# Kernel optimization log

Hardware: AMD Instinct MI355X
Metric: run time of the kernel (lower is better)

Reference implementation:

```python
import jax, jax.numpy as jnp
import numpy as np

B, N_PROP = 2, 512
C_FEAT, FH, FW = 256, 200, 200
NUM_CLASSES, NUM_STAGES = 81, 3
POOL, SR, SCALE = 7, 2, 0.25
IMG_H, IMG_W = 800.0, 800.0
FC_DIM = 1024
IN_DIM = C_FEAT * POOL * POOL
STDS = ((0.1, 0.1, 0.2, 0.2), (0.05, 0.05, 0.1, 0.1), (0.033, 0.033, 0.067, 0.067))
CLIP_VAL = float(np.log(1000.0 / 16))
SCORE_T, NMS_T, DETS, PRE_NMS = 0.05, 0.5, 100, 2048


def bilinear(f, y, x):
    # f: [C,H,W]; y,x: [M] sample coords (torchvision roi_align bilinear rules)
    H, W = f.shape[1], f.shape[2]
    valid = (y > -1.0) & (y < H) & (x > -1.0) & (x < W)
    y = jnp.clip(y, 0.0, H - 1.0)
    x = jnp.clip(x, 0.0, W - 1.0)
    y0 = jnp.floor(y).astype(jnp.int32)
    x0 = jnp.floor(x).astype(jnp.int32)
    y1 = jnp.minimum(y0 + 1, H - 1)
    x1 = jnp.minimum(x0 + 1, W - 1)
    ly, lx = y - y0, x - x0
    hy, hx = 1.0 - ly, 1.0 - lx
    v = (hy * hx) * f[:, y0, x0] + (hy * lx) * f[:, y0, x1] \
      + (ly * hx) * f[:, y1, x0] + (ly * lx) * f[:, y1, x1]
    return v * valid  # [C,M]


def roi_align(f, rois):
    # f: [C,H,W], rois: [N,4] image coords -> [N,C,POOL,POOL]
    b = rois * SCALE
    x1, y1, x2, y2 = b[:, 0], b[:, 1], b[:, 2], b[:, 3]
    rw = jnp.maximum(x2 - x1, 1.0)
    rh = jnp.maximum(y2 - y1, 1.0)
    bw, bh = rw / POOL, rh / POOL
    p = jnp.arange(POOL, dtype=f.dtype)
    s = (jnp.arange(SR, dtype=f.dtype) + 0.5) / SR
    gy = y1[:, None, None] + (p[None, :, None] + s[None, None, :]) * bh[:, None, None]  # [N,P,SR]
    gx = x1[:, None, None] + (p[None, :, None] + s[None, None, :]) * bw[:, None, None]
    n = rois.shape[0]
    yy = jnp.broadcast_to(gy[:, :, :, None, None], (n, POOL, SR, POOL, SR))
    xx = jnp.broadcast_to(gx[:, None, None, :, :], (n, POOL, SR, POOL, SR))
    vals = bilinear(f, yy.reshape(-1), xx.reshape(-1))  # [C, N*P*SR*P*SR]
    vals = vals.reshape(f.shape[0], n, POOL, SR, POOL, SR).mean(axis=(3, 5))
    return vals.transpose(1, 0, 2, 3)


def decode_clip(props, deltas, stds):
    px1, py1, px2, py2 = props[:, 0], props[:, 1], props[:, 2], props[:, 3]
    pw = jnp.maximum(px2 - px1, 1e-6)
    ph = jnp.maximum(py2 - py1, 1e-6)
    px = px1 + 0.5 * pw
    py = py1 + 0.5 * ph
    wx, wy, ww, wh = stds
    dx = deltas[:, 0] * wx
    dy = deltas[:, 1] * wy
    dw = jnp.minimum(deltas[:, 2] * ww, CLIP_VAL)
    dh = jnp.minimum(deltas[:, 3] * wh, CLIP_VAL)
    gx = dx * pw + px
    gy = dy * ph + py
    gw = jnp.exp(dw) * pw
    gh = jnp.exp(dh) * ph
    return jnp.stack([jnp.clip(gx - 0.5 * gw, 0.0, IMG_W),
                      jnp.clip(gy - 0.5 * gh, 0.0, IMG_H),
                      jnp.clip(gx + 0.5 * gw, 0.0, IMG_W),
                      jnp.clip(gy + 0.5 * gh, 0.0, IMG_H)], axis=1)


def box_iou(a, b):
    area_a = (a[:, 2] - a[:, 0]) * (a[:, 3] - a[:, 1])
    area_b = (b[:, 2] - b[:, 0]) * (b[:, 3] - b[:, 1])
    lt = jnp.maximum(a[:, None, :2], b[None, :, :2])
    rb = jnp.minimum(a[:, None, 2:], b[None, :, 2:])
    wh = jnp.maximum(rb - lt, 0.0)
    inter = wh[..., 0] * wh[..., 1]
    return inter / (area_a[:, None] + area_b[None, :] - inter + 1e-12)


def postprocess(boxes, probs):
    # boxes [N,4], probs [N,NUM_CLASSES] -> fixed-size padded detections
    n = boxes.shape[0]
    ws = boxes[:, 2] - boxes[:, 0]
    hs = boxes[:, 3] - boxes[:, 1]
    ok = (ws >= 1.0) & (hs >= 1.0)  # remove_small_boxes(min_size=1.0)
    fg = probs[:, 1:]               # drop background (class 0)
    sc = jnp.where((fg > SCORE_T) & ok[:, None], fg, -1.0).reshape(-1)  # [N*(C-1)]
    labels = jnp.broadcast_to(jnp.arange(1, NUM_CLASSES, dtype=jnp.int32)[None, :],
                              (n, NUM_CLASSES - 1)).reshape(-1)
    bflat = jnp.broadcast_to(boxes[:, None, :], (n, NUM_CLASSES - 1, 4)).reshape(-1, 4)
    vals, idx = jax.lax.top_k(sc, PRE_NMS)  # fixed-size candidate cap, sorted desc
    bsel = bflat[idx]
    lsel = labels[idx]
    # batched_nms trick: offset boxes per label so classes never overlap
    off = bsel + (lsel.astype(bsel.dtype) * (jnp.max(bsel) + 1.0))[:, None]
    iou = box_iou(off, off)
    valid = vals > 0.0
    ar = jnp.arange(PRE_NMS)
    def body(i, keep):
        sup = (iou[i] > NMS_T) & keep[i]
        return keep & ~(sup & (ar > i))
    keep = jax.lax.fori_loop(0, PRE_NMS, body, valid)
    order = jnp.argsort(jnp.where(keep, ar, PRE_NMS + ar))[:DETS]  # kept first, score order
    kv = keep[order]
    out_boxes = jnp.where(kv[:, None], bsel[order], 0.0)
    out_scores = jnp.where(kv, vals[order], 0.0)
    out_labels = jnp.where(kv, lsel[order], 0)
    return out_boxes, out_scores, out_labels


def cascade_forward(features, proposals, W1, b1, W2, b2, Wc, bc, Wr, br):
    cur = proposals  # [B,N,4]
    logits = None
    for s in range(NUM_STAGES):
        pooled = jax.vmap(roi_align)(features, cur)  # [B,N,C,P,P]
        x = pooled.reshape(B * N_PROP, IN_DIM)
        h = jax.nn.relu(x @ W1[s] + b1[s])
        h = jax.nn.relu(h @ W2[s] + b2[s])
        logits = h @ Wc[s] + bc[s]
        deltas = (h @ Wr[s] + br[s]).reshape(B, N_PROP, 4)
        stds = STDS[s]
        cur = jax.vmap(lambda p, d: decode_clip(p, d, stds))(cur, deltas)
    probs = jax.nn.softmax(logits, axis=-1).reshape(B, N_PROP, NUM_CLASSES)
    return jax.vmap(postprocess)(cur, probs)


def setup_inputs() -> dict:
    key = jax.random.key(0)
    ks = jax.random.split(key, 12)
    features = jax.random.normal(ks[0], (B, C_FEAT, FH, FW), jnp.float32)
    cx = jax.random.uniform(ks[1], (B, N_PROP), minval=0.0, maxval=IMG_W)
    cy = jax.random.uniform(ks[2], (B, N_PROP), minval=0.0, maxval=IMG_H)
    w = jax.random.uniform(ks[3], (B, N_PROP), minval=16.0, maxval=256.0)
    h = jax.random.uniform(ks[4], (B, N_PROP), minval=16.0, maxval=256.0)
    proposals = jnp.stack([jnp.clip(cx - w / 2, 0.0, IMG_W), jnp.clip(cy - h / 2, 0.0, IMG_H),
                           jnp.clip(cx + w / 2, 0.0, IMG_W), jnp.clip(cy + h / 2, 0.0, IMG_H)],
                          axis=-1)
    def lin(k, fan_in, shape):
        return jax.random.normal(k, shape, jnp.float32) / np.sqrt(fan_in).astype(np.float32)
    W1 = lin(ks[5], IN_DIM, (NUM_STAGES, IN_DIM, FC_DIM))
    W2 = lin(ks[6], FC_DIM, (NUM_STAGES, FC_DIM, FC_DIM))
    Wc = lin(ks[7], FC_DIM, (NUM_STAGES, FC_DIM, NUM_CLASSES))
    Wr = lin(ks[8], FC_DIM, (NUM_STAGES, FC_DIM, 4)) * 0.5
    b1 = jnp.zeros((NUM_STAGES, FC_DIM), jnp.float32)
    b2 = jnp.zeros((NUM_STAGES, FC_DIM), jnp.float32)
    bc = jnp.zeros((NUM_STAGES, NUM_CLASSES), jnp.float32)
    br = jnp.zeros((NUM_STAGES, 4), jnp.float32)
    return {"features": features, "proposals": proposals, "W1": W1, "b1": b1,
            "W2": W2, "b2": b2, "Wc": Wc, "bc": bc, "Wr": Wr, "br": br}


def reference(features, proposals, W1, b1, W2, b2, Wc, bc, Wr, br):
    return cascade_forward(features, proposals, W1, b1, W2, b2, Wc, bc, Wr, br)
```

## Files before the change

kernel.cpp:

```cpp
#include <hip/hip_runtime.h>
#include <float.h>
#include <math.h>

#define NB 2
#define NPROP 512
#define NROI 1024
#define CFEAT 256
#define FH 200
#define FW 200
#define HWSZ 40000
#define INDIM 12544
#define FCD 1024
#define NCLS 81
#define NCAND 40960
#define CAP 4096
#define NSEL 2048
#define DETS 100
#define CLIPV 4.135166556742356f

#define KKT1 392
#define KKT2 32
#define SPLITK 8

typedef __attribute__((ext_vector_type(8))) short short8v;
typedef __attribute__((ext_vector_type(8))) unsigned short ushort8v;
typedef __attribute__((ext_vector_type(4))) float float4v;

__device__ __forceinline__ unsigned short f2bf(float x) {
    unsigned u = __float_as_uint(x);
    unsigned r = (u + 0x7fffu + ((u >> 16) & 1u)) >> 16;
    return (unsigned short)r;
}
__device__ __forceinline__ float bf2f(unsigned short b) {
    return __uint_as_float(((unsigned)b) << 16);
}
__device__ __forceinline__ void split3(float x, unsigned short& h, unsigned short& m, unsigned short& l) {
    h = f2bf(x);
    float r1 = x - bf2f(h);
    m = f2bf(r1);
    float r2 = r1 - bf2f(m);
    l = f2bf(r2);
}

__device__ __forceinline__ void gload_lds16(const void* g, void* l) {
    __builtin_amdgcn_global_load_lds((const __attribute__((address_space(1))) unsigned int*)g,
                                     (__attribute__((address_space(3))) unsigned int*)l, 16, 0, 0);
}

__device__ __forceinline__ int swz8k(int o) {
    return o ^ ((((o >> 6) ^ (o >> 8)) & 3) << 4);
}

__global__ void zero_ints_k(int* p, int n) {
    int i = blockIdx.x * blockDim.x + threadIdx.x;
    if (i < n) p[i] = 0;
}

__global__ __launch_bounds__(256) void transpose_k(const float* __restrict__ in, float* __restrict__ out) {
    __shared__ float tile[32][33];
    int b = blockIdx.z;
    int hw0 = blockIdx.x * 32;
    int c0 = blockIdx.y * 32;
    int tx = threadIdx.x;
    int ty = threadIdx.y;
#pragma unroll
    for (int i = 0; i < 32; i += 8)
        tile[ty + i][tx] = in[((size_t)(b * CFEAT + c0 + ty + i)) * HWSZ + hw0 + tx];
    __syncthreads();
#pragma unroll
    for (int i = 0; i < 32; i += 8)
        out[((size_t)b * HWSZ + hw0 + ty + i) * CFEAT + c0 + tx] = tile[tx][ty + i];
}

template<bool TRANS>
__device__ __forceinline__ float bil_sample(const float* __restrict__ feat, int b, int c,
                                            float yy, float xx) {
    bool valid = (yy > -1.f) && (yy < (float)FH) && (xx > -1.f) && (xx < (float)FW);
    float yc = fminf(fmaxf(yy, 0.f), (float)(FH - 1));
    float xc = fminf(fmaxf(xx, 0.f), (float)(FW - 1));
    int y0 = (int)floorf(yc), x0 = (int)floorf(xc);
    int y1i = min(y0 + 1, FH - 1), x1i = min(x0 + 1, FW - 1);
    float ly = yc - (float)y0, lx = xc - (float)x0;
    float hy = 1.f - ly, hx = 1.f - lx;
    float v00, v01, v10, v11;
    if (TRANS) {
        const float* base = feat + (size_t)b * HWSZ * CFEAT;
        v00 = base[((size_t)(y0 * FW + x0)) * CFEAT + c];
        v01 = base[((size_t)(y0 * FW + x1i)) * CFEAT + c];
        v10 = base[((size_t)(y1i * FW + x0)) * CFEAT + c];
        v11 = base[((size_t)(y1i * FW + x1i)) * CFEAT + c];
    } else {
        const float* base = feat + ((size_t)(b * CFEAT + c)) * HWSZ;
        v00 = base[y0 * FW + x0];
        v01 = base[y0 * FW + x1i];
        v10 = base[y1i * FW + x0];
        v11 = base[y1i * FW + x1i];
    }
    float v = hy * hx * v00 + hy * lx * v01 + ly * hx * v10 + ly * lx * v11;
    return valid ? v : 0.f;
}

template<bool TRANS>
__global__ __launch_bounds__(256) void roi_k(const float* __restrict__ feat,
                                             const float* __restrict__ boxes,
                                             float* __restrict__ xout) {
    int pp = blockIdx.x, r = blockIdx.y, c = threadIdx.x;
    int b = r >> 9;
    const float* bx = boxes + (size_t)r * 4;
    float x1 = bx[0] * 0.25f, y1 = bx[1] * 0.25f, x2 = bx[2] * 0.25f, y2 = bx[3] * 0.25f;
    float rw = fmaxf(x2 - x1, 1.0f), rh = fmaxf(y2 - y1, 1.0f);
    float bw = rw / 7.0f, bh = rh / 7.0f;
    int py = pp / 7, px = pp % 7;
    float acc = 0.f;
#pragma unroll
    for (int sy = 0; sy < 2; ++sy)
#pragma unroll
        for (int sx = 0; sx < 2; ++sx)
            acc += bil_sample<TRANS>(feat, b, c,
                                     y1 + ((float)py + 0.25f + 0.5f * (float)sy) * bh,
                                     x1 + ((float)px + 0.25f + 0.5f * (float)sx) * bw);
    xout[(size_t)r * INDIM + pp * 256 + c] = acc * 0.25f;
}

template<bool TRANS>
__global__ __launch_bounds__(256) void roi_split_k(const float* __restrict__ feat,
                                                   const float* __restrict__ boxes,
                                                   unsigned short* __restrict__ Ap) {
    int r = blockIdx.x;
    int c = threadIdx.x;
    int b = r >> 9;
    const float* bx = boxes + (size_t)r * 4;
    float x1 = bx[0] * 0.25f, y1 = bx[1] * 0.25f, x2 = bx[2] * 0.25f, y2 = bx[3] * 0.25f;
    float rw = fmaxf(x2 - x1, 1.0f), rh = fmaxf(y2 - y1, 1.0f);
    float bw = rw / 7.0f, bh = rh / 7.0f;
    int mt = r >> 7, rr = r & 127;
    size_t pstr = (size_t)8 * KKT1 * 4096;
    for (int pp = 0; pp < 49; ++pp) {
        int py = pp / 7, px = pp % 7;
        float acc = 0.f;
#pragma unroll
        for (int sy = 0; sy < 2; ++sy)
#pragma unroll
            for (int sx = 0; sx < 2; ++sx)
                acc += bil_sample<TRANS>(feat, b, c,
                                         y1 + ((float)py + 0.25f + 0.5f * (float)sy) * bh,
                                         x1 + ((float)px + 0.25f + 0.5f * (float)sx) * bw);
        acc *= 0.25f;
        unsigned short h, m, l;
        split3(acc, h, m, l);
        int k = pp * 256 + c;
        int kk = k >> 5;
        size_t tile = ((size_t)mt * KKT1 + kk) * 4096 + rr * 32 + (k & 31);
        Ap[tile] = h;
        Ap[tile + pstr] = m;
        Ap[tile + 2 * pstr] = l;
    }
}

template<bool PERM>
__global__ __launch_bounds__(256) void wsplit_k(const float* __restrict__ W,
                                                unsigned short* __restrict__ out, int kkT) {
    __shared__ float tf[32][132];
    int nt = blockIdx.x, kk = blockIdx.y;
    int t = threadIdx.x;
    int kloc = t >> 3;
    int f4 = t & 7;
    int krow;
    if (PERM) krow = ((kk & 7) * 32 + kloc) * 49 + (kk >> 3);
    else krow = kk * 32 + kloc;
    const float* src = W + (size_t)krow * 1024 + nt * 128;
#pragma unroll
    for (int q = 0; q < 4; ++q) {
        float4 v = *(const float4*)(src + (f4 + q * 8) * 4);
        *(float4*)&tf[kloc][(f4 + q * 8) * 4] = v;
    }
    __syncthreads();
    int r = t >> 1;
    size_t tileBase = ((size_t)nt * kkT + kk) * 4096;
    size_t pstr = (size_t)8 * kkT * 4096;
#pragma unroll
    for (int cc = 0; cc < 2; ++cc) {
        int c = (t & 1) * 2 + cc;
        ushort8v hv, mv, lv;
#pragma unroll
        for (int e = 0; e < 8; ++e) {
            unsigned short h, m, l;
            split3(tf[c * 8 + e][r], h, m, l);
            hv[e] = h; mv[e] = m; lv[e] = l;
        }
        size_t o = tileBase + r * 32 + c * 8;
        *(ushort8v*)&out[o] = hv;
        *(ushort8v*)&out[o + pstr] = mv;
        *(ushort8v*)&out[o + 2 * pstr] = lv;
    }
}

#define TERM16(AF) { _Pragma("unroll") for (int i = 0; i < 4; ++i) _Pragma("unroll") \
    for (int j = 0; j < 4; ++j) acc[i][j] = __builtin_amdgcn_mfma_f32_16x16x32_bf16(AF[i], bf[j], acc[i][j], 0, 0, 0); }

__global__ __launch_bounds__(256) void gemm_mfma_k(const unsigned short* __restrict__ Ap,
                                                   const unsigned short* __restrict__ Bp,
                                                   float* __restrict__ partial,
                                                   int kkT, int kkPer) {
    __shared__ unsigned short sA[3][4096];
    __shared__ unsigned short sB[3][4096];
    int tid = threadIdx.x;
    int phys = blockIdx.x;
    int logical = (phys & 7) * (gridDim.x >> 3) + (phys >> 3);
    int xy = logical & 63;
    int ck = logical >> 6;
    int mt = xy & 7, nt = xy >> 3;
    int kk0 = ck * kkPer;
    size_t pstrB = (size_t)8 * kkT * 4096 * 2;
    const char* aBase = (const char*)(Ap + (size_t)mt * kkT * 4096);
    const char* bBase = (const char*)(Bp + (size_t)nt * kkT * 4096);

    float4v acc[4][4];
#pragma unroll
    for (int i = 0; i < 4; ++i)
#pragma unroll
        for (int j = 0; j < 4; ++j) acc[i][j] = (float4v){0.f, 0.f, 0.f, 0.f};

    int lane = tid & 63, wv = tid >> 6;
    int wr = wv >> 1, wc = wv & 1;
    int ln = lane & 15;
    int q = lane >> 4;
    int qs = (q ^ (ln ^ (ln >> 2))) & 3;
    int aoffE = (wr * 64 + ln) * 32 + qs * 8;
    int boffE = (wc * 64 + ln) * 32 + qs * 8;

    int o0 = tid * 16;
    int o1 = o0 + 4096;
    int s0 = swz8k(o0);
    int s1 = swz8k(o1);

    for (int kk = kk0; kk < kk0 + kkPer; ++kk) {
        const char* at = aBase + (size_t)kk * 8192;
        const char* bt = bBase + (size_t)kk * 8192;
#pragma unroll
        for (int p = 0; p < 3; ++p) {
            gload_lds16(at + (size_t)p * pstrB + s0, (char*)sA[p] + o0);
            gload_lds16(at + (size_t)p * pstrB + s1, (char*)sA[p] + o1);
            gload_lds16(bt + (size_t)p * pstrB + s0, (char*)sB[p] + o0);
            gload_lds16(bt + (size_t)p * pstrB + s1, (char*)sB[p] + o1);
        }
        __syncthreads();
        short8v af[3][4];
#pragma unroll
        for (int p = 0; p < 3; ++p)
#pragma unroll
            for (int f = 0; f < 4; ++f)
                af[p][f] = *(const short8v*)&sA[p][aoffE + f * 512];
        short8v bf[4];
#pragma unroll
        for (int f = 0; f < 4; ++f) bf[f] = *(const short8v*)&sB[0][boffE + f * 512];
        TERM16(af[0]); TERM16(af[1]); TERM16(af[2]);
#pragma unroll
        for (int f = 0; f < 4; ++f) bf[f] = *(const short8v*)&sB[1][boffE + f * 512];
        TERM16(af[0]); TERM16(af[1]);
#pragma unroll
        for (int f = 0; f < 4; ++f) bf[f] = *(const short8v*)&sB[2][boffE + f * 512];
        TERM16(af[0]);
        __syncthreads();
    }
    float* outp = partial + ((size_t)ck << 20);
    int row0 = mt * 128 + wr * 64 + (lane >> 4) * 4;
    int col = nt * 128 + wc * 64 + ln;
#pragma unroll
    for (int i = 0; i < 4; ++i)
#pragma unroll
        for (int j = 0; j < 4; ++j)
#pragma unroll
            for (int qq = 0; qq < 4; ++qq)
                outp[(size_t)(row0 + i * 16 + qq) * 1024 + col + j * 16] = acc[i][j][qq];
}

template<int MODE>
__global__ void reduce8_k(const float* __restrict__ partial, const float* __restrict__ bias,
                          unsigned short* __restrict__ planes, float* __restrict__ fout) {
    int i = blockIdx.x * 256 + threadIdx.x;
    float s = 0.f;
#pragma unroll
    for (int c = 0; c < SPLITK; ++c) s += partial[((size_t)c << 20) + i];
    s += bias[i & 1023];
    s = fmaxf(s, 0.f);
    if (MODE == 0) {
        int m = i >> 10, n = i & 1023;
        int mt = m >> 7, rr = m & 127, kk = n >> 5;
        unsigned short h, mm_, l;
        split3(s, h, mm_, l);
        size_t tile = ((size_t)mt * KKT2 + kk) * 4096 + rr * 32 + (n & 31);
        size_t pstr = (size_t)8 * KKT2 * 4096;
        planes[tile] = h;
        planes[tile + pstr] = mm_;
        planes[tile + 2 * pstr] = l;
    } else {
        fout[i] = s;
    }
}

template<bool PERM>
__global__ __launch_bounds__(256) void gemm_k(const float* __restrict__ A,
                                              const float* __restrict__ Bm,
                                              float* __restrict__ partial,
                                              int K_total, int Kchunk) {
    const int M = 1024, N = 1024;
    __shared__ float As[2][16][128];
    __shared__ float Bs[2][16][64];
    int tid = threadIdx.x;
    int mb = blockIdx.x & 7;
    int nb = blockIdx.x >> 3;
    int ck = blockIdx.y;
    int k0 = ck * Kchunk;
    int am = tid >> 1;
    int ak = (tid & 1) * 8;
    int bk = tid >> 4;
    int bn = (tid & 15) * 4;
    int ty = tid >> 4, tx = tid & 15;
    const float* Aptr = A + (size_t)(mb * 128 + am) * K_total + k0 + ak;

    float acc[8][4];
#pragma unroll
    for (int i = 0; i < 8; ++i)
#pragma unroll
        for (int j = 0; j < 4; ++j) acc[i][j] = 0.f;

    auto bRowPtr = [&](int kk) -> const float* {
        int row = PERM ? ((kk & 255) * 49 + (kk >> 8)) : kk;
        return Bm + (size_t)row * N + nb * 64 + bn;
    };

    int T = Kchunk / 16;
    float4 a0 = *(const float4*)(Aptr);
    float4 a1 = *(const float4*)(Aptr + 4);
    float4 b0 = *(const float4*)bRowPtr(k0 + bk);
    As[0][ak + 0][am] = a0.x; As[0][ak + 1][am] = a0.y; As[0][ak + 2][am] = a0.z; As[0][ak + 3][am] = a0.w;
    As[0][ak + 4][am] = a1.x; As[0][ak + 5][am] = a1.y; As[0][ak + 6][am] = a1.z; As[0][ak + 7][am] = a1.w;
    *(float4*)&Bs[0][bk][bn] = b0;
    __syncthreads();

    int p = 0;
    for (int t = 0; t < T; ++t) {
        if (t + 1 < T) {
            a0 = *(const float4*)(Aptr + (t + 1) * 16);
            a1 = *(const float4*)(Aptr + (t + 1) * 16 + 4);
            b0 = *(const float4*)bRowPtr(k0 + (t + 1) * 16 + bk);
        }
#pragma unroll
        for (int k = 0; k < 16; ++k) {
            float4 av0 = *(const float4*)&As[p][k][ty * 8];
            float4 av1 = *(const float4*)&As[p][k][ty * 8 + 4];
            float4 bv = *(const float4*)&Bs[p][k][tx * 4];
            float ar[8] = {av0.x, av0.y, av0.z, av0.w, av1.x, av1.y, av1.z, av1.w};
            float br_[4] = {bv.x, bv.y, bv.z, bv.w};
#pragma unroll
            for (int i = 0; i < 8; ++i)
#pragma unroll
                for (int j = 0; j < 4; ++j) acc[i][j] = fmaf(ar[i], br_[j], acc[i][j]);
        }
        if (t + 1 < T) {
            __syncthreads();
            int qb = 1 - p;
            As[qb][ak + 0][am] = a0.x; As[qb][ak + 1][am] = a0.y; As[qb][ak + 2][am] = a0.z; As[qb][ak + 3][am] = a0.w;
            As[qb][ak + 4][am] = a1.x; As[qb][ak + 5][am] = a1.y; As[qb][ak + 6][am] = a1.z; As[qb][ak + 7][am] = a1.w;
            *(float4*)&Bs[qb][bk][bn] = b0;
            __syncthreads();
            p = qb;
        }
    }
    float* out = partial + ((size_t)ck * M + mb * 128 + ty * 8) * N + nb * 64 + tx * 4;
#pragma unroll
    for (int i = 0; i < 8; ++i) {
        float4 v = make_float4(acc[i][0], acc[i][1], acc[i][2], acc[i][3]);
        *(float4*)(out + (size_t)i * N) = v;
    }
}

__global__ void reduce4_k(const float* __restrict__ partial, const float* __restrict__ bias,
                          float* __restrict__ out) {
    const int MN = 1024 * 1024;
    int i = blockIdx.x * 256 + threadIdx.x;
    if (i >= MN) return;
    float s = partial[i] + partial[(size_t)MN + i] + partial[(size_t)2 * MN + i] + partial[(size_t)3 * MN + i];
    s += bias[i & 1023];
    out[i] = fmaxf(s, 0.f);
}

__global__ __launch_bounds__(128) void head_k(const float* __restrict__ h,
                                              const float* __restrict__ Wc, const float* __restrict__ bc,
                                              const float* __restrict__ Wr, const float* __restrict__ br,
                                              float* __restrict__ logits, float* __restrict__ deltas,
                                              int write_logits) {
    __shared__ float hs[1024];
    int m = blockIdx.x;
    int tid = threadIdx.x;
    const float4* hp = (const float4*)(h + (size_t)m * 1024);
    ((float4*)hs)[tid] = hp[tid];
    ((float4*)hs)[tid + 128] = hp[tid + 128];
    __syncthreads();
    int j = tid;
    if (j < 85) {
        bool is_cls = j < 81;
        const float* Wp = is_cls ? Wc : Wr;
        int stride = is_cls ? 81 : 4;
        int col = is_cls ? j : j - 81;
        float s0 = 0.f, s1 = 0.f, s2 = 0.f, s3 = 0.f;
        for (int k = 0; k < 1024; k += 4) {
            s0 = fmaf(hs[k + 0], Wp[(k + 0) * stride + col], s0);
            s1 = fmaf(hs[k + 1], Wp[(k + 1) * stride + col], s1);
            s2 = fmaf(hs[k + 2], Wp[(k + 2) * stride + col], s2);
            s3 = fmaf(hs[k + 3], Wp[(k + 3) * stride + col], s3);
        }
        float s = (s0 + s1) + (s2 + s3);
        if (is_cls) {
            if (write_logits) logits[(size_t)m * NCLS + col] = s + bc[col];
        } else {
            deltas[(size_t)m * 4 + col] = s + br[col];
        }
    }
}

__global__ void decode_k(const float* __restrict__ prev, const float* __restrict__ deltas,
                         float* __restrict__ nxt, float wx, float wy, float ww, float wh) {
    int r = blockIdx.x * 256 + threadIdx.x;
    if (r >= NROI) return;
    const float* p = prev + (size_t)r * 4;
    const float* d = deltas + (size_t)r * 4;
    float px1 = p[0], py1 = p[1], px2 = p[2], py2 = p[3];
    float pw = fmaxf(px2 - px1, 1e-6f), ph = fmaxf(py2 - py1, 1e-6f);
    float pcx = px1 + 0.5f * pw, pcy = py1 + 0.5f * ph;
    float dx = d[0] * wx, dy = d[1] * wy;
    float dw = fminf(d[2] * ww, CLIPV);
    float dh = fminf(d[3] * wh, CLIPV);
    float gx = dx * pw + pcx, gy = dy * ph + pcy;
    float gw = expf(dw) * pw, gh = expf(dh) * ph;
    nxt[(size_t)r * 4 + 0] = fminf(fmaxf(gx - 0.5f * gw, 0.f), 800.f);
    nxt[(size_t)r * 4 + 1] = fminf(fmaxf(gy - 0.5f * gh, 0.f), 800.f);
    nxt[(size_t)r * 4 + 2] = fminf(fmaxf(gx + 0.5f * gw, 0.f), 800.f);
    nxt[(size_t)r * 4 + 3] = fminf(fmaxf(gy + 0.5f * gh, 0.f), 800.f);
}

__global__ __launch_bounds__(128) void softmax_k(const float* __restrict__ logits, float* __restrict__ probs) {
    __shared__ float red[128];
    int m = blockIdx.x;
    int tid = threadIdx.x;
    float v = (tid < NCLS) ? logits[(size_t)m * NCLS + tid] : -FLT_MAX;
    red[tid] = v;
    __syncthreads();
    for (int o = 64; o; o >>= 1) {
        if (tid < o) red[tid] = fmaxf(red[tid], red[tid + o]);
        __syncthreads();
    }
    float mx = red[0];
    __syncthreads();
    float e = (tid < NCLS) ? expf(v - mx) : 0.f;
    red[tid] = e;
    __syncthreads();
    for (int o = 64; o; o >>= 1) {
        if (tid < o) red[tid] += red[tid + o];
        __syncthreads();
    }
    float s = red[0];
    if (tid < NCLS) probs[(size_t)m * NCLS + tid] = e / s;
}

__global__ void build_scores_k(const float* __restrict__ probs, const float* __restrict__ boxes,
                               float* __restrict__ sc, int* __restrict__ vcount) {
    int f = blockIdx.x * 256 + threadIdx.x;
    if (f >= NB * NCAND) return;
    int b = f / NCAND, ff = f % NCAND;
    int rr = ff / 80, cls = ff % 80 + 1;
    int row = b * NPROP + rr;
    const float* bx = boxes + (size_t)row * 4;
    bool ok = (bx[2] - bx[0] >= 1.f) && (bx[3] - bx[1] >= 1.f);
    float p = probs[(size_t)row * NCLS + cls];
    float s = (p > 0.05f && ok) ? p : -1.0f;
    sc[f] = s;
    if (s > 0.f) atomicAdd(&vcount[b], 1);
}

__global__ __launch_bounds__(1024) void find_pivot_k(const float* __restrict__ sc,
                                                     const int* __restrict__ vcount,
                                                     float* __restrict__ pivot) {
    int b = blockIdx.x;
    const float* s = sc + (size_t)b * NCAND;
    __shared__ int tot;
    int V = vcount[b];
    if (V <= CAP) {
        if (threadIdx.x == 0) pivot[b] = 0.f;
        return;
    }
    unsigned u = 0;
    for (int bit = 30; bit >= 0; --bit) {
        unsigned cand = u | (1u << bit);
        float cf = __uint_as_float(cand);
        if (threadIdx.x == 0) tot = 0;
        __syncthreads();
        int cnt = 0;
        for (int i = threadIdx.x; i < NCAND; i += 1024) cnt += (s[i] >= cf) ? 1 : 0;
        for (int o = 32; o; o >>= 1) cnt += __shfl_down(cnt, o);
        if ((threadIdx.x & 63) == 0) atomicAdd(&tot, cnt);
        __syncthreads();
        if (tot >= NSEL) u = cand;
        __syncthreads();
    }
    if (threadIdx.x == 0) pivot[b] = __uint_as_float(u);
}

__global__ void compact_k(const float* __restrict__ sc, const float* __restrict__ pivot,
                          float* __restrict__ ckey, int* __restrict__ cidx, int* __restrict__ ccount) {
    int f = blockIdx.x * 256 + threadIdx.x;
    if (f >= NB * NCAND) return;
    int b = f / NCAND, ff = f % NCAND;
    float s = sc[f];
    float pv = pivot[b];
    if (s > 0.f && s >= pv) {
        int slot = atomicAdd(&ccount[b], 1);
        if (slot < CAP) {
            ckey[(size_t)b * CAP + slot] = s;
            cidx[(size_t)b * CAP + slot] = ff;
        }
    }
}

__global__ __launch_bounds__(1024) void sort_select_k(const float* __restrict__ ckey,
                                                      const int* __restrict__ cidx,
                                                      const int* __restrict__ ccount,
                                                      const float* __restrict__ boxes,
                                                      float* __restrict__ selb, float* __restrict__ seloff,
                                                      float* __restrict__ selsc, int* __restrict__ sellab,
                                                      unsigned long long* __restrict__ vmask) {
    int b = blockIdx.x;
    __shared__ float ks[CAP];
    __shared__ int is[CAP];
    __shared__ float rmax[1024];
    int cnt = min(ccount[b], CAP);
    for (int i = threadIdx.x; i < CAP; i += 1024) {
        if (i < cnt) {
            ks[i] = ckey[(size_t)b * CAP + i];
            is[i] = cidx[(size_t)b * CAP + i];
        } else {
            ks[i] = -FLT_MAX;
            is[i] = 0x7FFFFFFF;
        }
    }
    __syncthreads();
    for (int k = 2; k <= CAP; k <<= 1) {
        for (int j = k >> 1; j > 0; j >>= 1) {
            for (int t = threadIdx.x; t < CAP; t += 1024) {
                int l = t ^ j;
                if (l > t) {
                    bool up = ((t & k) == 0);
                    float a = ks[t], bb = ks[l];
                    int ia = is[t], ib = is[l];
                    bool a_first = (a > bb) || (a == bb && ia < ib);
                    bool doswap = up ? !a_first : a_first;
                    if (doswap) {
                        ks[t] = bb; ks[l] = a;
                        is[t] = ib; is[l] = ia;
                    }
                }
            }
            __syncthreads();
        }
    }
    float lm = -FLT_MAX;
    for (int i = threadIdx.x; i < NSEL; i += 1024) {
        if (ks[i] > 0.f) {
            const float* bb = boxes + (size_t)(b * NPROP + is[i] / 80) * 4;
            lm = fmaxf(lm, fmaxf(fmaxf(bb[0], bb[1]), fmaxf(bb[2], bb[3])));
        }
    }
    rmax[threadIdx.x] = lm;
    __syncthreads();
    for (int o = 512; o; o >>= 1) {
        if (threadIdx.x < o) rmax[threadIdx.x] = fmaxf(rmax[threadIdx.x], rmax[threadIdx.x + o]);
        __syncthreads();
    }
    float maxb = (rmax[0] > -FLT_MAX) ? rmax[0] : 0.f;
    __syncthreads();
    for (int pass = 0; pass < 2; ++pass) {
        int i = pass * 1024 + threadIdx.x;
        bool v = ks[i] > 0.f;
        int idx = is[i];
        int rr = idx / 80;
        int cls = idx % 80 + 1;
        float b0 = 0.f, b1 = 0.f, b2 = 0.f, b3 = 0.f, offv = 0.f;
        if (v) {
            const float* bb = boxes + (size_t)(b * NPROP + rr) * 4;
            b0 = bb[0]; b1 = bb[1]; b2 = bb[2]; b3 = bb[3];
            offv = (maxb + 1.f) * (float)cls;
        }
        float* sb = selb + ((size_t)b * NSEL + i) * 4;
        sb[0] = b0; sb[1] = b1; sb[2] = b2; sb[3] = b3;
        float* so = seloff + ((size_t)b * NSEL + i) * 4;
        so[0] = b0 + offv; so[1] = b1 + offv; so[2] = b2 + offv; so[3] = b3 + offv;
        selsc[(size_t)b * NSEL + i] = v ? ks[i] : 0.f;
        sellab[(size_t)b * NSEL + i] = cls;
        unsigned long long m = __ballot(v);
        if ((threadIdx.x & 63) == 0) vmask[b * 32 + pass * 16 + (threadIdx.x >> 6)] = m;
    }
}

__global__ __launch_bounds__(256) void sup_k(const float* __restrict__ seloff,
                                             unsigned long long* __restrict__ sup) {
    int b = blockIdx.y;
    int wave = threadIdx.x >> 6;
    int lane = threadIdx.x & 63;
    int pair = blockIdx.x * 4 + wave;
    int i = pair >> 5;
    int w = pair & 31;
    int j = w * 64 + lane;
    const float* oi = seloff + ((size_t)b * NSEL + i) * 4;
    const float* oj = seloff + ((size_t)b * NSEL + j) * 4;
    float ax1 = oi[0], ay1 = oi[1], ax2 = oi[2], ay2 = oi[3];
    float bx1 = oj[0], by1 = oj[1], bx2 = oj[2], by2 = oj[3];
    float areaA = (ax2 - ax1) * (ay2 - ay1);
    float areaB = (bx2 - bx1) * (by2 - by1);
    float ltx = fmaxf(ax1, bx1), lty = fmaxf(ay1, by1);
    float rbx = fminf(ax2, bx2), rby = fminf(ay2, by2);
    float iw = fmaxf(rbx - ltx, 0.f), ih = fmaxf(rby - lty, 0.f);
    float inter = iw * ih;
    float iou = inter / (areaA + areaB - inter + 1e-12f);
    unsigned long long m = __ballot(iou > 0.5f);
    if (lane == 0) sup[((size_t)b * NSEL + i) * 32 + w] = m;
}

__global__ __launch_bounds__(256) void nms_scan_k(const unsigned long long* __restrict__ vmask,
                                                  const unsigned long long* __restrict__ sup,
                                                  const float* __restrict__ selb,
                                                  const float* __restrict__ selsc,
                                                  const int* __restrict__ sellab,
                                                  float* __restrict__ out) {
    int b = blockIdx.x;
    __shared__ unsigned long long keepw[32];
    __shared__ int pref[33];
    int tid = threadIdx.x;
    if (tid < 64) {
        int lane = tid;
        unsigned long long kw = (lane < 32) ? vmask[b * 32 + lane] : 0ull;
        for (int i = 0; i < NSEL; ++i) {
            int wi = i >> 6;
            unsigned long long wv = __shfl(kw, wi);
            if ((wv >> (i & 63)) & 1ull) {
                if (lane < 32) {
                    unsigned long long row = sup[((size_t)b * NSEL + i) * 32 + lane];
                    unsigned long long mask;
                    if (lane > wi) mask = ~0ull;
                    else if (lane == wi) mask = ((i & 63) == 63) ? 0ull : (~0ull << ((i & 63) + 1));
                    else mask = 0ull;
                    kw &= ~(row & mask);
                }
            }
        }
        if (lane < 32) keepw[lane] = kw;
    }
    __syncthreads();
    if (tid == 0) {
        int s = 0;
        for (int w = 0; w < 32; ++w) { pref[w] = s; s += __popcll(keepw[w]); }
        pref[32] = s;
    }
    __syncthreads();
    for (int i = tid; i < 600; i += 256) {
        if (i < 400) out[b * 400 + i] = 0.f;
        else if (i < 500) out[800 + b * 100 + (i - 400)] = 0.f;
        else out[1000 + b * 100 + (i - 500)] = 0.f;
    }
    __syncthreads();
    for (int e = tid; e < NSEL; e += 256) {
        int w = e >> 6;
        unsigned long long kw = keepw[w];
        if ((kw >> (e & 63)) & 1ull) {
            int rank = pref[w] + __popcll(kw & ((1ull << (e & 63)) - 1ull));
            if (rank < DETS) {
                const float* sb = selb + ((size_t)b * NSEL + e) * 4;
                out[b * 400 + rank * 4 + 0] = sb[0];
                out[b * 400 + rank * 4 + 1] = sb[1];
                out[b * 400 + rank * 4 + 2] = sb[2];
                out[b * 400 + rank * 4 + 3] = sb[3];
                out[800 + b * 100 + rank] = selsc[(size_t)b * NSEL + e];
                out[1000 + b * 100 + rank] = (float)sellab[(size_t)b * NSEL + e];
            }
        }
    }
}

extern "C" void kernel_launch(void* const* d_in, const int* in_sizes, int n_in,
                              void* d_out, int out_size, void* d_ws, size_t ws_size,
                              hipStream_t stream) {
    const float* features = (const float*)d_in[0];
    const float* proposals = (const float*)d_in[1];
    const float* W1 = (const float*)d_in[2];
    const float* b1 = (const float*)d_in[3];
    const float* W2 = (const float*)d_in[4];
    const float* b2 = (const float*)d_in[5];
    const float* Wc = (const float*)d_in[6];
    const float* bc = (const float*)d_in[7];
    const float* Wr = (const float*)d_in[8];
    const float* br = (const float*)d_in[9];

    char* ws = (char*)d_ws;
    size_t off = 0;
    auto alloc = [&](size_t bytes) -> void* {
        void* p = ws + off;
        off += (bytes + 255) & ~(size_t)255;
        return p;
    };

    float* logits = (float*)alloc((size_t)NROI * NCLS * 4);
    float* probs = (float*)alloc((size_t)NROI * NCLS * 4);
    float* deltas = (float*)alloc((size_t)NROI * 4 * 4);
    float* cur1 = (float*)alloc((size_t)NROI * 4 * 4);
    float* cur2 = (float*)alloc((size_t)NROI * 4 * 4);
    float* cur3 = (float*)alloc((size_t)NROI * 4 * 4);
    float* sc = (float*)alloc((size_t)NB * NCAND * 4);
    float* ckey = (float*)alloc((size_t)NB * CAP * 4);
    int* cidx = (int*)alloc((size_t)NB * CAP * 4);
    int* counters = (int*)alloc(256);
    float* pivot = (float*)(counters + 4);
    float* selb = (float*)alloc((size_t)NB * NSEL * 4 * 4);
    float* seloff = (float*)alloc((size_t)NB * NSEL * 4 * 4);
    float* selsc = (float*)alloc((size_t)NB * NSEL * 4);
    int* sellab = (int*)alloc((size_t)NB * NSEL * 4);
    unsigned long long* vmask = (unsigned long long*)alloc((size_t)NB * 32 * 8);
    unsigned long long* sup = (unsigned long long*)alloc((size_t)NB * NSEL * 32 * 8);

    const float stds[3][4] = {{0.1f, 0.1f, 0.2f, 0.2f},
                              {0.05f, 0.05f, 0.1f, 0.1f},
                              {0.033f, 0.033f, 0.067f, 0.067f}};
    float* curbufs[3] = {cur1, cur2, cur3};
    const float* curp = proposals;

    size_t planes1 = (size_t)3 * 8 * KKT1 * 4096 * 2;
    size_t planes2 = (size_t)3 * 8 * KKT2 * 4096 * 2;
    size_t need_new = planes1 * 2 + planes2 * 2 +
                      (size_t)SPLITK * 1024 * 1024 * 4 + (size_t)1024 * 1024 * 4 +
                      (size_t)NB * HWSZ * CFEAT * 4 + 4096;

    zero_ints_k<<<1, 64, 0, stream>>>(counters, 4);

    if (off + need_new <= ws_size) {
        unsigned short* Ap1 = (unsigned short*)alloc(planes1);
        unsigned short* Bp1 = (unsigned short*)alloc(planes1);
        unsigned short* h1p = (unsigned short*)alloc(planes2);
        unsigned short* W2Tp = (unsigned short*)alloc(planes2);
        float* partial = (float*)alloc((size_t)SPLITK * 1024 * 1024 * 4);
        float* h2 = (float*)alloc((size_t)1024 * 1024 * 4);
        float* featT = (float*)alloc((size_t)NB * HWSZ * CFEAT * 4);

        transpose_k<<<dim3(1250, 8, 2), dim3(32, 8), 0, stream>>>(features, featT);

        for (int s = 0; s < 3; ++s) {
            roi_split_k<true><<<dim3(NROI), 256, 0, stream>>>(featT, curp, Ap1);
            wsplit_k<true><<<dim3(8, KKT1), 256, 0, stream>>>(W1 + (size_t)s * INDIM * FCD, Bp1, KKT1);
            gemm_mfma_k<<<dim3(64 * SPLITK), 256, 0, stream>>>(Ap1, Bp1, partial, KKT1, KKT1 / SPLITK);
            reduce8_k<0><<<4096, 256, 0, stream>>>(partial, b1 + s * FCD, h1p, nullptr);
            wsplit_k<false><<<dim3(8, KKT2), 256, 0, stream>>>(W2 + (size_t)s * FCD * FCD, W2Tp, KKT2);
            gemm_mfma_k<<<dim3(64 * SPLITK), 256, 0, stream>>>(h1p, W2Tp, partial, KKT2, KKT2 / SPLITK);
            reduce8_k<1><<<4096, 256, 0, stream>>>(partial, b2 + s * FCD, nullptr, h2);
            head_k<<<1024, 128, 0, stream>>>(h2, Wc + (size_t)s * FCD * NCLS, bc + s * NCLS,
                                             Wr + (size_t)s * FCD * 4, br + s * 4,
                                             logits, deltas, (s == 2) ? 1 : 0);
            decode_k<<<4, 256, 0, stream>>>(curp, deltas, curbufs[s],
                                            stds[s][0], stds[s][1], stds[s][2], stds[s][3]);
            curp = curbufs[s];
        }
    } else {
        float* x = (float*)alloc((size_t)NROI * INDIM * 4);
        float* partial = (float*)alloc((size_t)4 * 1024 * 1024 * 4);
        float* h1 = (float*)alloc((size_t)NROI * FCD * 4);
        float* h2 = (float*)alloc((size_t)NROI * FCD * 4);
        float* featT = (float*)alloc((size_t)NB * HWSZ * CFEAT * 4);
        bool use_trans = (off <= ws_size);

        if (use_trans)
            transpose_k<<<dim3(1250, 8, 2), dim3(32, 8), 0, stream>>>(features, featT);

        for (int s = 0; s < 3; ++s) {
            if (use_trans)
                roi_k<true><<<dim3(49, 1024), 256, 0, stream>>>(featT, curp, x);
            else
                roi_k<false><<<dim3(49, 1024), 256, 0, stream>>>(features, curp, x);
            gemm_k<true><<<dim3(128, 4), 256, 0, stream>>>(x, W1 + (size_t)s * INDIM * FCD, partial, INDIM, 3136);
            reduce4_k<<<4096, 256, 0, stream>>>(partial, b1 + s * FCD, h1);
            gemm_k<false><<<dim3(128, 4), 256, 0, stream>>>(h1, W2 + (size_t)s * FCD * FCD, partial, FCD, 256);
            reduce4_k<<<4096, 256, 0, stream>>>(partial, b2 + s * FCD, h2);
            head_k<<<1024, 128, 0, stream>>>(h2, Wc + (size_t)s * FCD * NCLS, bc + s * NCLS,
                                             Wr + (size_t)s * FCD * 4, br + s * 4,
                                             logits, deltas, (s == 2) ? 1 : 0);
            decode_k<<<4, 256, 0, stream>>>(curp, deltas, curbufs[s],
                                            stds[s][0], stds[s][1], stds[s][2], stds[s][3]);
            curp = curbufs[s];
        }
    }

    softmax_k<<<1024, 128, 0, stream>>>(logits, probs);
    build_scores_k<<<320, 256, 0, stream>>>(probs, curp, sc, counters);
    find_pivot_k<<<2, 1024, 0, stream>>>(sc, counters, pivot);
    compact_k<<<320, 256, 0, stream>>>(sc, pivot, ckey, cidx, counters + 2);
    sort_select_k<<<2, 1024, 0, stream>>>(ckey, cidx, counters + 2, curp, selb, seloff, selsc, sellab, vmask);
    sup_k<<<dim3(16384, 2), 256, 0, stream>>>(seloff, sup);
    nms_scan_k<<<2, 256, 0, stream>>>(vmask, sup, selb, selsc, sellab, (float*)d_out);
}
```

Measured before the change: 1.235 ms.

## Vectorize ROI align, move head to MFMA, raise split-K, skip empty NMS rows

ROI align now handles two ROIs per block. Each thread gathers float4 channels and writes packed bf16 split planes. The classification/regression head no longer uses a scalar head_k kernel: it runs as an MFMA GEMM on a split-bf16 packed head weight, followed by a small finalize kernel. The first GEMM's split-K factor goes from 8 to 14 when the workspace allows it, and the NMS suppression kernel skips IoU work for rows whose selected score is zero. Together these target memory gather inefficiency, scalar head compute and GEMM occupancy, at the cost of more workspace and extra launches.

```diff
diff --git a/kernel.cpp b/kernel.cpp
--- a/kernel.cpp
+++ b/kernel.cpp
@@ -20,7 +20,6 @@
 
 #define KKT1 392
 #define KKT2 32
-#define SPLITK 8
 
 typedef __attribute__((ext_vector_type(8))) short short8v;
 typedef __attribute__((ext_vector_type(8))) unsigned short ushort8v;
@@ -122,12 +121,14 @@
     xout[(size_t)r * INDIM + pp * 256 + c] = acc * 0.25f;
 }
 
-template<bool TRANS>
-__global__ __launch_bounds__(256) void roi_split_k(const float* __restrict__ feat,
-                                                   const float* __restrict__ boxes,
-                                                   unsigned short* __restrict__ Ap) {
-    int r = blockIdx.x;
-    int c = threadIdx.x;
+__global__ __launch_bounds__(256) void roi_split4_k(const float* __restrict__ feat,
+                                                    const float* __restrict__ boxes,
+                                                    unsigned short* __restrict__ Ap) {
+    int tid = threadIdx.x;
+    int g = tid >> 7;
+    int binhalf = (tid >> 6) & 1;
+    int cl = tid & 63;
+    int r = blockIdx.x * 2 + g;
     int b = r >> 9;
     const float* bx = boxes + (size_t)r * 4;
     float x1 = bx[0] * 0.25f, y1 = bx[1] * 0.25f, x2 = bx[2] * 0.25f, y2 = bx[3] * 0.25f;
@@ -135,25 +136,47 @@
     float bw = rw / 7.0f, bh = rh / 7.0f;
     int mt = r >> 7, rr = r & 127;
     size_t pstr = (size_t)8 * KKT1 * 4096;
-    for (int pp = 0; pp < 49; ++pp) {
+    const float* base = feat + (size_t)b * HWSZ * CFEAT;
+    for (int pp = binhalf; pp < 49; pp += 2) {
         int py = pp / 7, px = pp % 7;
-        float acc = 0.f;
-#pragma unroll
-        for (int sy = 0; sy < 2; ++sy)
-#pragma unroll
-            for (int sx = 0; sx < 2; ++sx)
-                acc += bil_sample<TRANS>(feat, b, c,
-                                         y1 + ((float)py + 0.25f + 0.5f * (float)sy) * bh,
-                                         x1 + ((float)px + 0.25f + 0.5f * (float)sx) * bw);
-        acc *= 0.25f;
-        unsigned short h, m, l;
-        split3(acc, h, m, l);
-        int k = pp * 256 + c;
-        int kk = k >> 5;
-        size_t tile = ((size_t)mt * KKT1 + kk) * 4096 + rr * 32 + (k & 31);
-        Ap[tile] = h;
-        Ap[tile + pstr] = m;
-        Ap[tile + 2 * pstr] = l;
+        float ax = 0.f, ay = 0.f, az = 0.f, aw = 0.f;
+#pragma unroll
+        for (int sy = 0; sy < 2; ++sy) {
+#pragma unroll
+            for (int sx = 0; sx < 2; ++sx) {
+                float yy = y1 + ((float)py + 0.25f + 0.5f * (float)sy) * bh;
+                float xx = x1 + ((float)px + 0.25f + 0.5f * (float)sx) * bw;
+                bool valid = (yy > -1.f) && (yy < (float)FH) && (xx > -1.f) && (xx < (float)FW);
+                float yc = fminf(fmaxf(yy, 0.f), (float)(FH - 1));
+                float xc = fminf(fmaxf(xx, 0.f), (float)(FW - 1));
+                int y0 = (int)floorf(yc), x0 = (int)floorf(xc);
+                int y1i = min(y0 + 1, FH - 1), x1i = min(x0 + 1, FW - 1);
+                float ly = yc - (float)y0, lx = xc - (float)x0;
+                float hy = 1.f - ly, hx = 1.f - lx;
+                float w00 = hy * hx, w01 = hy * lx, w10 = ly * hx, w11 = ly * lx;
+                if (!valid) { w00 = w01 = w10 = w11 = 0.f; }
+                float4 v00 = ((const float4*)(base + (size_t)(y0 * FW + x0) * CFEAT))[cl];
+                float4 v01 = ((const float4*)(base + (size_t)(y0 * FW + x1i) * CFEAT))[cl];
+                float4 v10 = ((const float4*)(base + (size_t)(y1i * FW + x0) * CFEAT))[cl];
+                float4 v11 = ((const float4*)(base + (size_t)(y1i * FW + x1i) * CFEAT))[cl];
+                ax += w00 * v00.x + w01 * v01.x + w10 * v10.x + w11 * v11.x;
+                ay += w00 * v00.y + w01 * v01.y + w10 * v10.y + w11 * v11.y;
+                az += w00 * v00.z + w01 * v01.z + w10 * v10.z + w11 * v11.z;
+                aw += w00 * v00.w + w01 * v01.w + w10 * v10.w + w11 * v11.w;
+            }
+        }
+        ax *= 0.25f; ay *= 0.25f; az *= 0.25f; aw *= 0.25f;
+        ushort4 h4, m4, l4;
+        split3(ax, h4.x, m4.x, l4.x);
+        split3(ay, h4.y, m4.y, l4.y);
+        split3(az, h4.z, m4.z, l4.z);
+        split3(aw, h4.w, m4.w, l4.w);
+        int k0 = pp * 256 + cl * 4;
+        int kk = k0 >> 5;
+        size_t tile = ((size_t)mt * KKT1 + kk) * 4096 + rr * 32 + (k0 & 31);
+        *(ushort4*)&Ap[tile] = h4;
+        *(ushort4*)&Ap[tile + pstr] = m4;
+        *(ushort4*)&Ap[tile + 2 * pstr] = l4;
     }
 }
 
@@ -195,23 +218,47 @@
     }
 }
 
+__global__ __launch_bounds__(256) void wsplit_head_k(const float* __restrict__ Wc,
+                                                     const float* __restrict__ Wr,
+                                                     unsigned short* __restrict__ out) {
+    int kk = blockIdx.x, t = threadIdx.x;
+    int r = t >> 1;
+    int k0 = (t & 1) * 16;
+    size_t pstr = (size_t)KKT2 * 4096;
+    for (int e = 0; e < 16; ++e) {
+        int k = k0 + e;
+        int krow = kk * 32 + k;
+        float v = 0.f;
+        if (r < 81) v = Wc[(size_t)krow * 81 + r];
+        else if (r < 85) v = Wr[(size_t)krow * 4 + (r - 81)];
+        unsigned short h, m, l;
+        split3(v, h, m, l);
+        size_t o = (size_t)kk * 4096 + r * 32 + k;
+        out[o] = h;
+        out[o + pstr] = m;
+        out[o + 2 * pstr] = l;
+    }
+}
+
 #define TERM16(AF) { _Pragma("unroll") for (int i = 0; i < 4; ++i) _Pragma("unroll") \
     for (int j = 0; j < 4; ++j) acc[i][j] = __builtin_amdgcn_mfma_f32_16x16x32_bf16(AF[i], bf[j], acc[i][j], 0, 0, 0); }
 
 __global__ __launch_bounds__(256) void gemm_mfma_k(const unsigned short* __restrict__ Ap,
                                                    const unsigned short* __restrict__ Bp,
                                                    float* __restrict__ partial,
-                                                   int kkT, int kkPer) {
+                                                   int kkT, int kkPer, int NT, int N) {
     __shared__ unsigned short sA[3][4096];
     __shared__ unsigned short sB[3][4096];
     int tid = threadIdx.x;
     int phys = blockIdx.x;
     int logical = (phys & 7) * (gridDim.x >> 3) + (phys >> 3);
-    int xy = logical & 63;
-    int ck = logical >> 6;
+    int tpc = 8 * NT;
+    int xy = logical % tpc;
+    int ck = logical / tpc;
     int mt = xy & 7, nt = xy >> 3;
     int kk0 = ck * kkPer;
-    size_t pstrB = (size_t)8 * kkT * 4096 * 2;
+    size_t pstrA = (size_t)8 * kkT * 4096 * 2;
+    size_t pstrB = (size_t)NT * kkT * 4096 * 2;
     const char* aBase = (const char*)(Ap + (size_t)mt * kkT * 4096);
     const char* bBase = (const char*)(Bp + (size_t)nt * kkT * 4096);
 
@@ -239,8 +286,8 @@
         const char* bt = bBase + (size_t)kk * 8192;
 #pragma unroll
         for (int p = 0; p < 3; ++p) {
-            gload_lds16(at + (size_t)p * pstrB + s0, (char*)sA[p] + o0);
-            gload_lds16(at + (size_t)p * pstrB + s1, (char*)sA[p] + o1);
+            gload_lds16(at + (size_t)p * pstrA + s0, (char*)sA[p] + o0);
+            gload_lds16(at + (size_t)p * pstrA + s1, (char*)sA[p] + o1);
             gload_lds16(bt + (size_t)p * pstrB + s0, (char*)sB[p] + o0);
             gload_lds16(bt + (size_t)p * pstrB + s1, (char*)sB[p] + o1);
         }
@@ -263,7 +310,7 @@
         TERM16(af[0]);
         __syncthreads();
     }
-    float* outp = partial + ((size_t)ck << 20);
+    float* outp = partial + (size_t)ck * 1024 * N;
     int row0 = mt * 128 + wr * 64 + (lane >> 4) * 4;
     int col = nt * 128 + wc * 64 + ln;
 #pragma unroll
@@ -272,30 +319,42 @@
         for (int j = 0; j < 4; ++j)
 #pragma unroll
             for (int qq = 0; qq < 4; ++qq)
-                outp[(size_t)(row0 + i * 16 + qq) * 1024 + col + j * 16] = acc[i][j][qq];
-}
-
-template<int MODE>
+                outp[(size_t)(row0 + i * 16 + qq) * N + col + j * 16] = acc[i][j][qq];
+}
+
+template<int NS>
 __global__ void reduce8_k(const float* __restrict__ partial, const float* __restrict__ bias,
-                          unsigned short* __restrict__ planes, float* __restrict__ fout) {
+                          unsigned short* __restrict__ planes) {
     int i = blockIdx.x * 256 + threadIdx.x;
     float s = 0.f;
 #pragma unroll
-    for (int c = 0; c < SPLITK; ++c) s += partial[((size_t)c << 20) + i];
+    for (int c = 0; c < NS; ++c) s += partial[((size_t)c << 20) + i];
     s += bias[i & 1023];
     s = fmaxf(s, 0.f);
-    if (MODE == 0) {
-        int m = i >> 10, n = i & 1023;
-        int mt = m >> 7, rr = m & 127, kk = n >> 5;
-        unsigned short h, mm_, l;
-        split3(s, h, mm_, l);
-        size_t tile = ((size_t)mt * KKT2 + kk) * 4096 + rr * 32 + (n & 31);
-        size_t pstr = (size_t)8 * KKT2 * 4096;
-        planes[tile] = h;
-        planes[tile + pstr] = mm_;
-        planes[tile + 2 * pstr] = l;
+    int m = i >> 10, n = i & 1023;
+    int mt = m >> 7, rr = m & 127, kk = n >> 5;
+    unsigned short h, mm_, l;
+    split3(s, h, mm_, l);
+    size_t tile = ((size_t)mt * KKT2 + kk) * 4096 + rr * 32 + (n & 31);
+    size_t pstr = (size_t)8 * KKT2 * 4096;
+    planes[tile] = h;
+    planes[tile + pstr] = mm_;
+    planes[tile + 2 * pstr] = l;
+}
+
+__global__ void head_fin_k(const float* __restrict__ partial, const float* __restrict__ bc,
+                           const float* __restrict__ br, float* __restrict__ logits,
+                           float* __restrict__ deltas, int write_logits) {
+    int idx = blockIdx.x * 256 + threadIdx.x;
+    if (idx >= 1024 * 85) return;
+    int m = idx / 85, col = idx - m * 85;
+    float s = 0.f;
+#pragma unroll
+    for (int c = 0; c < 8; ++c) s += partial[(size_t)c * 131072 + m * 128 + col];
+    if (col < 81) {
+        if (write_logits) logits[(size_t)m * NCLS + col] = s + bc[col];
     } else {
-        fout[i] = s;
+        deltas[(size_t)m * 4 + (col - 81)] = s + br[col - 81];
     }
 }
 
@@ -603,6 +662,7 @@
 }
 
 __global__ __launch_bounds__(256) void sup_k(const float* __restrict__ seloff,
+                                             const float* __restrict__ selsc,
                                              unsigned long long* __restrict__ sup) {
     int b = blockIdx.y;
     int wave = threadIdx.x >> 6;
@@ -611,18 +671,21 @@
     int i = pair >> 5;
     int w = pair & 31;
     int j = w * 64 + lane;
-    const float* oi = seloff + ((size_t)b * NSEL + i) * 4;
-    const float* oj = seloff + ((size_t)b * NSEL + j) * 4;
-    float ax1 = oi[0], ay1 = oi[1], ax2 = oi[2], ay2 = oi[3];
-    float bx1 = oj[0], by1 = oj[1], bx2 = oj[2], by2 = oj[3];
-    float areaA = (ax2 - ax1) * (ay2 - ay1);
-    float areaB = (bx2 - bx1) * (by2 - by1);
-    float ltx = fmaxf(ax1, bx1), lty = fmaxf(ay1, by1);
-    float rbx = fminf(ax2, bx2), rby = fminf(ay2, by2);
-    float iw = fmaxf(rbx - ltx, 0.f), ih = fmaxf(rby - lty, 0.f);
-    float inter = iw * ih;
-    float iou = inter / (areaA + areaB - inter + 1e-12f);
-    unsigned long long m = __ballot(iou > 0.5f);
+    unsigned long long m = 0;
+    if (selsc[(size_t)b * NSEL + i] > 0.f) {
+        const float* oi = seloff + ((size_t)b * NSEL + i) * 4;
+        const float* oj = seloff + ((size_t)b * NSEL + j) * 4;
+        float ax1 = oi[0], ay1 = oi[1], ax2 = oi[2], ay2 = oi[3];
+        float bx1 = oj[0], by1 = oj[1], bx2 = oj[2], by2 = oj[3];
+        float areaA = (ax2 - ax1) * (ay2 - ay1);
+        float areaB = (bx2 - bx1) * (by2 - by1);
+        float ltx = fmaxf(ax1, bx1), lty = fmaxf(ay1, by1);
+        float rbx = fminf(ax2, bx2), rby = fminf(ay2, by2);
+        float iw = fmaxf(rbx - ltx, 0.f), ih = fmaxf(rby - lty, 0.f);
+        float inter = iw * ih;
+        float iou = inter / (areaA + areaB - inter + 1e-12f);
+        m = __ballot(iou > 0.5f);
+    }
     if (lane == 0) sup[((size_t)b * NSEL + i) * 32 + w] = m;
 }
 
@@ -734,34 +797,46 @@
 
     size_t planes1 = (size_t)3 * 8 * KKT1 * 4096 * 2;
     size_t planes2 = (size_t)3 * 8 * KKT2 * 4096 * 2;
-    size_t need_new = planes1 * 2 + planes2 * 2 +
-                      (size_t)SPLITK * 1024 * 1024 * 4 + (size_t)1024 * 1024 * 4 +
-                      (size_t)NB * HWSZ * CFEAT * 4 + 4096;
+    size_t planesH = (size_t)3 * 1 * KKT2 * 4096 * 2;
+    auto mfma_need = [&](int sk) {
+        return planes1 * 2 + planes2 * 3 + planesH +
+               (size_t)sk * (1 << 20) * 4 +
+               (size_t)NB * HWSZ * CFEAT * 4 + 65536;
+    };
+    int SK1 = 0;
+    if (off + mfma_need(14) <= ws_size) SK1 = 14;
+    else if (off + mfma_need(8) <= ws_size) SK1 = 8;
 
     zero_ints_k<<<1, 64, 0, stream>>>(counters, 4);
 
-    if (off + need_new <= ws_size) {
+    if (SK1 > 0) {
         unsigned short* Ap1 = (unsigned short*)alloc(planes1);
         unsigned short* Bp1 = (unsigned short*)alloc(planes1);
         unsigned short* h1p = (unsigned short*)alloc(planes2);
         unsigned short* W2Tp = (unsigned short*)alloc(planes2);
-        float* partial = (float*)alloc((size_t)SPLITK * 1024 * 1024 * 4);
-        float* h2 = (float*)alloc((size_t)1024 * 1024 * 4);
+        unsigned short* h2p = (unsigned short*)alloc(planes2);
+        unsigned short* Whp = (unsigned short*)alloc(planesH);
+        float* partial = (float*)alloc((size_t)SK1 * (1 << 20) * 4);
         float* featT = (float*)alloc((size_t)NB * HWSZ * CFEAT * 4);
 
         transpose_k<<<dim3(1250, 8, 2), dim3(32, 8), 0, stream>>>(features, featT);
 
         for (int s = 0; s < 3; ++s) {
-            roi_split_k<true><<<dim3(NROI), 256, 0, stream>>>(featT, curp, Ap1);
+            roi_split4_k<<<dim3(NROI / 2), 256, 0, stream>>>(featT, curp, Ap1);
             wsplit_k<true><<<dim3(8, KKT1), 256, 0, stream>>>(W1 + (size_t)s * INDIM * FCD, Bp1, KKT1);
-            gemm_mfma_k<<<dim3(64 * SPLITK), 256, 0, stream>>>(Ap1, Bp1, partial, KKT1, KKT1 / SPLITK);
-            reduce8_k<0><<<4096, 256, 0, stream>>>(partial, b1 + s * FCD, h1p, nullptr);
+            gemm_mfma_k<<<dim3(64 * SK1), 256, 0, stream>>>(Ap1, Bp1, partial, KKT1, KKT1 / SK1, 8, 1024);
+            if (SK1 == 14)
+                reduce8_k<14><<<4096, 256, 0, stream>>>(partial, b1 + s * FCD, h1p);
+            else
+                reduce8_k<8><<<4096, 256, 0, stream>>>(partial, b1 + s * FCD, h1p);
             wsplit_k<false><<<dim3(8, KKT2), 256, 0, stream>>>(W2 + (size_t)s * FCD * FCD, W2Tp, KKT2);
-            gemm_mfma_k<<<dim3(64 * SPLITK), 256, 0, stream>>>(h1p, W2Tp, partial, KKT2, KKT2 / SPLITK);
-            reduce8_k<1><<<4096, 256, 0, stream>>>(partial, b2 + s * FCD, nullptr, h2);
-            head_k<<<1024, 128, 0, stream>>>(h2, Wc + (size_t)s * FCD * NCLS, bc + s * NCLS,
-                                             Wr + (size_t)s * FCD * 4, br + s * 4,
-                                             logits, deltas, (s == 2) ? 1 : 0);
+            gemm_mfma_k<<<dim3(512), 256, 0, stream>>>(h1p, W2Tp, partial, KKT2, 4, 8, 1024);
+            reduce8_k<8><<<4096, 256, 0, stream>>>(partial, b2 + s * FCD, h2p);
+            wsplit_head_k<<<dim3(KKT2), 256, 0, stream>>>(Wc + (size_t)s * FCD * NCLS,
+                                                          Wr + (size_t)s * FCD * 4, Whp);
+            gemm_mfma_k<<<dim3(64), 256, 0, stream>>>(h2p, Whp, partial, KKT2, 4, 1, 128);
+            head_fin_k<<<dim3(340), 256, 0, stream>>>(partial, bc + s * NCLS, br + s * 4,
+                                                      logits, deltas, (s == 2) ? 1 : 0);
             decode_k<<<4, 256, 0, stream>>>(curp, deltas, curbufs[s],
                                             stds[s][0], stds[s][1], stds[s][2], stds[s][3]);
             curp = curbufs[s];
@@ -800,6 +875,6 @@
     find_pivot_k<<<2, 1024, 0, stream>>>(sc, counters, pivot);
     compact_k<<<320, 256, 0, stream>>>(sc, pivot, ckey, cidx, counters + 2);
     sort_select_k<<<2, 1024, 0, stream>>>(ckey, cidx, counters + 2, curp, selb, seloff, selsc, sellab, vmask);
-    sup_k<<<dim3(16384, 2), 256, 0, stream>>>(seloff, sup);
+    sup_k<<<dim3(16384, 2), 256, 0, stream>>>(seloff, selsc, sup);
     nms_scan_k<<<2, 256, 0, stream>>>(vmask, sup, selb, selsc, sellab, (float*)d_out);
 }
```

Result: slower. 1.273 ms (+3.0%).
